# Optimization experiments

Measured on AMD Instinct MI355X. Metric: run time of the kernel, lower is better.

## Reference

```python
import jax, jax.numpy as jnp
import numpy as np

W_P, H_P = 2, 2  # patch rows, patch cols (size_of_patches[0])
HID, FC = 256, 1024

def _lstm_scan(x_seq, k, r, b):
    """Keras-style LSTM. x_seq: [T, N, Din] -> hidden states [T, N, H]."""
    N = x_seq.shape[1]
    H = r.shape[0]
    h0 = jnp.zeros((N, H), x_seq.dtype)
    c0 = jnp.zeros((N, H), x_seq.dtype)
    def step(carry, x):
        h, c = carry
        z = x @ k + h @ r + b  # [N, 4H], gate order i,f,g,o (keras)
        i, f, g, o = jnp.split(z, 4, axis=-1)
        c = jax.nn.sigmoid(f) * c + jax.nn.sigmoid(i) * jnp.tanh(g)
        h = jax.nn.sigmoid(o) * jnp.tanh(c)
        return (h, c), h
    _, hs = jax.lax.scan(step, (h0, c0), x_seq)
    return hs

def _bidir(x, k_f, r_f, b_f, k_b, r_b, b_b):
    # x: [T, N, D] -> [T, N, 2H]
    hf = _lstm_scan(x, k_f, r_f, b_f)
    hb = _lstm_scan(x[::-1], k_b, r_b, b_b)[::-1]
    return jnp.concatenate([hf, hb], axis=-1)

def reference(x, k_ud, r_ud, b_ud, k_du, r_du, b_du,
              k_lr, r_lr, b_lr, k_rl, r_rl, b_rl, Wd, bd):
    B, Hi, Wi, C = x.shape
    I, J = Hi // W_P, Wi // H_P
    # extract non-overlapping patches -> [B, I, J, w_p*h_p*C]
    p = x.reshape(B, I, W_P, J, H_P, C).transpose(0, 1, 3, 2, 4, 5)
    p = p.reshape(B, I, J, W_P * H_P * C)
    # vertical bidirectional sweep: sequence over rows i, batched over (B, J)
    v = p.transpose(1, 0, 2, 3).reshape(I, B * J, -1)          # [I, B*J, D]
    v = _bidir(v, k_ud, r_ud, b_ud, k_du, r_du, b_du)          # [I, B*J, 2H]
    v = v.reshape(I, B, J, -1).transpose(1, 0, 2, 3)           # [B, I, J, 2H]
    # horizontal bidirectional sweep: sequence over cols j, batched over (B, I)
    h = v.transpose(2, 0, 1, 3).reshape(J, B * I, -1)          # [J, B*I, 2H]
    h = _bidir(h, k_lr, r_lr, b_lr, k_rl, r_rl, b_rl)          # [J, B*I, 2H]
    h = h.reshape(J, B, I, -1).transpose(1, 2, 0, 3)           # [B, I, J, 2H]
    return jax.nn.relu(h @ Wd + bd)                            # [B, I, J, FC]

def setup_inputs() -> dict:
    key = jax.random.key(0)
    ks = jax.random.split(key, 16)
    D = W_P * H_P * 3
    def n(k, shape):
        return jax.random.normal(k, shape, dtype=jnp.float32) * 0.05
    inp = {"x": jax.random.normal(ks[0], (64, 64, 64, 3), dtype=jnp.float32)}
    for idx, (name, din) in enumerate([("ud", D), ("du", D), ("lr", 2 * HID), ("rl", 2 * HID)]):
        inp[f"k_{name}"] = n(ks[1 + 3 * idx], (din, 4 * HID))
        inp[f"r_{name}"] = n(ks[2 + 3 * idx], (HID, 4 * HID))
        inp[f"b_{name}"] = jnp.zeros((4 * HID,), jnp.float32)
    inp["Wd"] = n(ks[13], (2 * HID, FC))
    inp["bd"] = jnp.zeros((FC,), jnp.float32)
    return inp
```

## Files before the change

### kernel.cpp

```cpp
#include <hip/hip_runtime.h>
#include <math.h>
#include <stddef.h>
#include <stdint.h>


namespace {

typedef __bf16 bf16x8 __attribute__((ext_vector_type(8)));
typedef float f32x4 __attribute__((ext_vector_type(4)));
typedef __attribute__((address_space(1))) unsigned int as1_uint;
typedef __attribute__((address_space(3))) unsigned int as3_uint;

__device__ __forceinline__ float bf2f(ushort u) {
  return __builtin_bit_cast(float, (unsigned int)u << 16);
}
__device__ __forceinline__ ushort f2bf(float f) {
  unsigned int u = __builtin_bit_cast(unsigned int, f);
  u += 0x7fffu + ((u >> 16) & 1u);
  return (ushort)(u >> 16);
}
__device__ __forceinline__ unsigned int packbf(float a, float b) {
  return (unsigned int)f2bf(a) | ((unsigned int)f2bf(b) << 16);
}
__device__ __forceinline__ float sigm(float x) {
  return __fdividef(1.f, 1.f + __expf(-x));
}
__device__ __forceinline__ float tanh_(float x) {
  return 2.f * sigm(2.f * x) - 1.f;
}
__device__ __forceinline__ f32x4 mfma16(bf16x8 a, bf16x8 b, f32x4 c) {
  return __builtin_amdgcn_mfma_f32_16x16x32_bf16(a, b, c, 0, 0, 0);
}
__device__ __forceinline__ void load_lds16(const void* g, void* l) {
  __builtin_amdgcn_global_load_lds((const as1_uint*)g, (as3_uint*)l, 16, 0, 0);
}


__global__ __launch_bounds__(256) void transpose_all(
    const float* __restrict__ s0, const float* __restrict__ s1,
    const float* __restrict__ s2, ushort* __restrict__ d0,
    ushort* __restrict__ d1, ushort* __restrict__ d2) {
  const int which = blockIdx.y;
  const float* in = (which == 0) ? s0 : (which == 1) ? s1 : s2;
  ushort* out = (which == 0) ? d0 : (which == 1) ? d1 : d2;
  const int idx = blockIdx.x * 256 + threadIdx.x;
  const int n = idx >> 9, k = idx & 511;
  out[idx] = f2bf(in[k * 1024 + n]);
}

__global__ __launch_bounds__(256) void rfrag_all(
    const float* __restrict__ r0, const float* __restrict__ r1,
    const float* __restrict__ r2, const float* __restrict__ r3,
    ushort* __restrict__ out) {
  const int which = blockIdx.y;
  const float* r = (which == 0) ? r0 : (which == 1) ? r1 : (which == 2) ? r2 : r3;
  ushort* o = out + (size_t)which * 262144;
  const int id = blockIdx.x * 256 + threadIdx.x;
  const int lane = id & 63, kc = (id >> 6) & 7, tile = id >> 9;
  const int kbase = (kc << 5) + ((lane >> 4) << 3);
  const int col = (tile << 4) + (lane & 15);
  ushort tmp[8];
#pragma unroll
  for (int j = 0; j < 8; ++j) tmp[j] = f2bf(r[(size_t)(kbase + j) * 1024 + col]);
  *(uint4*)&o[(size_t)id << 3] = *(const uint4*)tmp;
}

__global__ __launch_bounds__(256) void kfragv_kernel(
    const float* __restrict__ k0, const float* __restrict__ b0,
    const float* __restrict__ k1, const float* __restrict__ b1,
    ushort* __restrict__ out) {
  const int dir = blockIdx.y;
  const int idx = blockIdx.x * 256 + threadIdx.x;
  const int lane = idx & 63;
  const int kbase = (lane >> 4) << 3;
  const int col = ((idx >> 6) << 4) + (lane & 15);
  const float* kw = dir ? k1 : k0;
  const float* bw = dir ? b1 : b0;
  ushort tmp[8];
#pragma unroll
  for (int j = 0; j < 8; ++j) {
    const int kidx = kbase + j;
    const float v = (kidx < 12) ? kw[kidx * 1024 + col]
                  : (kidx == 12) ? bw[col] : 0.f;
    tmp[j] = f2bf(v);
  }
  *(uint4*)&out[((size_t)dir * 4096 + idx) << 3] = *(const uint4*)tmp;
}

__global__ __launch_bounds__(512) void lstm_sweepV(
    const float* __restrict__ x, const ushort* __restrict__ kfragV,
    const uint4* __restrict__ rF, ushort* __restrict__ outbuf) {
  const int tid = threadIdx.x;
  const int lane = tid & 63, w = tid >> 6;
  const int l16 = lane & 15, kg = lane >> 4;
  const int rb = blockIdx.x, dir = (int)blockIdx.y;
  const int rowbase = rb << 4;
  const int bb = rb >> 1;
  const int jbase = (rb & 1) << 4;

  __shared__ ushort hbuf[2][4096];
  __shared__ uint4 kfr[4096];
  __shared__ ushort pb[2][512];

  const uint4* rFd = rF + (size_t)dir * 32768;

  for (int e = tid; e < 640; e += 512) {
    const int par = e / 320, rest = e - par * 320;
    const int row = rest / 20, c = 12 + rest % 20;
    pb[par][(row << 5) + c] = (c == 12) ? (ushort)0x3F80 : (ushort)0;
  }
  if (tid < 192) {
    const int row = tid / 12, d = tid - row * 12;
    const int pr = d / 6, rem = d - pr * 6, pc = rem / 3, c = rem - pc * 3;
    const int i0 = dir ? 31 : 0;
    const float v = x[((size_t)((bb * 64 + (i0 << 1) + pr) * 64) +
                       ((jbase + row) << 1) + pc) * 3 + c];
    pb[0][(row << 5) + d] = f2bf(v);
  }
#pragma unroll
  for (int i = 0; i < 8; ++i)
    load_lds16((const uint4*)kfragV + (size_t)dir * 4096 + tid + (i << 9),
               kfr + (tid - lane) + (i << 9));
  __syncthreads();

  float cst[2][4];
#pragma unroll
  for (int q = 0; q < 2; ++q)
#pragma unroll
    for (int r = 0; r < 4; ++r) cst[q][r] = 0.f;

  for (int t = 0; t < 32; ++t) {
    const int seq = dir ? (31 - t) : t;
    const ushort* hprev = hbuf[(t + 1) & 1];
    ushort* hnext = hbuf[t & 1];

    if (t) {
      const int seqP = dir ? (32 - t) : (t - 1);
      const int row = tid >> 5, c4o = tid & 31;
      const uint4 v = *(const uint4*)((const char*)hprev + row * 512 +
                                      ((c4o ^ (row & 7)) << 4));
      const int n = rowbase + row, b = n >> 5, sp = n & 31;
      *(uint4*)&outbuf[(((size_t)(b * 32 + seqP) * 32 + sp) << 9) +
                       (dir << 8) + (c4o << 3)] = v;
    }

    float pv = 0.f;
    if (t < 31 && tid < 192) {
      const int row = tid / 12, d = tid - row * 12;
      const int pr = d / 6, rem = d - pr * 6, pc = rem / 3, c = rem - pc * 3;
      const int iN = dir ? (30 - t) : (t + 1);
      pv = x[((size_t)((bb * 64 + (iN << 1) + pr) * 64) +
              ((jbase + row) << 1) + pc) * 3 + c];
    }

    const bf16x8 pf = __builtin_bit_cast(
        bf16x8, *(const uint4*)&pb[t & 1][(l16 << 5) + (kg << 3)]);
    f32x4 acc[2][4];
#pragma unroll
    for (int q = 0; q < 2; ++q) {
#pragma unroll
      for (int g = 0; g < 4; ++g) {
        const int tile = (g << 4) + (w << 1) + q;
        const bf16x8 kb = __builtin_bit_cast(bf16x8, kfr[(tile << 6) + lane]);
        acc[q][g] = mfma16(pf, kb, (f32x4){0.f, 0.f, 0.f, 0.f});
      }
    }

    if (t) {
#pragma unroll
      for (int q = 0; q < 2; ++q) {
        uint4 bfr[2][4];
#pragma unroll
        for (int g = 0; g < 4; ++g)
          bfr[0][g] = rFd[(size_t)(((g << 4) + (w << 1) + q) << 3) * 64 + lane];
#pragma unroll
        for (int kc = 0; kc < 8; ++kc) {
          const int cur = kc & 1;
          if (kc < 7) {
#pragma unroll
            for (int g = 0; g < 4; ++g)
              bfr[cur ^ 1][g] =
                  rFd[((size_t)(((g << 4) + (w << 1) + q) << 3) + kc + 1) * 64 +
                      lane];
          }
          const int c4 = (kc << 2) + kg;
          const uint4 a = *(const uint4*)((const char*)hprev + l16 * 512 +
                                          ((c4 ^ (l16 & 7)) << 4));
          const bf16x8 ab = __builtin_bit_cast(bf16x8, a);
#pragma unroll
          for (int g = 0; g < 4; ++g)
            acc[q][g] =
                mfma16(ab, __builtin_bit_cast(bf16x8, bfr[cur][g]), acc[q][g]);
        }
      }
    }

    if (t < 31 && tid < 192) {
      const int row = tid / 12, d = tid - row * 12;
      pb[(t + 1) & 1][(row << 5) + d] = f2bf(pv);
    }

#pragma unroll
    for (int q = 0; q < 2; ++q) {
      const int col = (w << 5) + (q << 4) + l16;
#pragma unroll
      for (int r = 0; r < 4; ++r) {
        const float zi = acc[q][0][r];
        const float zf = acc[q][1][r];
        const float zg = acc[q][2][r];
        const float zo = acc[q][3][r];
        const float cn = sigm(zf) * cst[q][r] + sigm(zi) * tanh_(zg);
        cst[q][r] = cn;
        const float hv = sigm(zo) * tanh_(cn);
        const int row = (kg << 2) + r;
        *(ushort*)((char*)hnext + row * 512 +
                   (((col >> 3) ^ (row & 7)) << 4) + ((col & 7) << 1)) =
            f2bf(hv);
      }
    }
    __syncthreads();
  }

  {
    const int seqP = dir ? 0 : 31;
    const ushort* hl = hbuf[1];
    const int row = tid >> 5, c4o = tid & 31;
    const uint4 v = *(const uint4*)((const char*)hl + row * 512 +
                                    ((c4o ^ (row & 7)) << 4));
    const int n = rowbase + row, b = n >> 5, sp = n & 31;
    *(uint4*)&outbuf[(((size_t)(b * 32 + seqP) * 32 + sp) << 9) + (dir << 8) +
                     (c4o << 3)] = v;
  }
}

__global__ __launch_bounds__(512) void lstm_sweep7(
    const uint4* __restrict__ Zf, const uint4* __restrict__ rF,
    ushort* __restrict__ outbuf, int vert) {
  const int tid = threadIdx.x;
  const int lane = tid & 63, w = tid >> 6;
  const int l16 = lane & 15, kg = lane >> 4;
  const int rb = blockIdx.x, dir = (int)blockIdx.y;
  const int rowbase = rb << 4;

  __shared__ ushort hbuf[2][4096];

  const uint4* rFd = rF + (size_t)dir * 32768;
  const uint4* zb = Zf + ((size_t)dir * 128 + rb) * 65536;

  float cst[2][4];
#pragma unroll
  for (int q = 0; q < 2; ++q)
#pragma unroll
    for (int r = 0; r < 4; ++r) cst[q][r] = 0.f;

  uint4 zA[2], zB[2];
  {
    const int seq0 = dir ? 31 : 0;
    zA[0] = zb[(size_t)(seq0 << 2) * 512 + tid];
    zA[1] = zb[(size_t)((seq0 << 2) + 1) * 512 + tid];
  }

  for (int t = 0; t < 32; ++t) {
    const ushort* hprev = hbuf[(t + 1) & 1];
    ushort* hnext = hbuf[t & 1];

    if (t) {
      const int seqP = dir ? (32 - t) : (t - 1);
      const int row = tid >> 5, c4 = tid & 31;
      const uint4 v = *(const uint4*)((const char*)hprev + row * 512 +
                                      ((c4 ^ (row & 7)) << 4));
      const int n = rowbase + row, b = n >> 5, sp = n & 31;
      const int X = vert ? seqP : sp, Y = vert ? sp : seqP;
      *(uint4*)&outbuf[(((size_t)(b * 32 + X) * 32 + Y) << 9) + (dir << 8) +
                       (c4 << 3)] = v;
    }

#pragma unroll
    for (int q = 0; q < 2; ++q) {
      uint4(&zc)[2] = (q == 0) ? zA : zB;
      uint4(&zn)[2] = (q == 0) ? zB : zA;

      f32x4 acc[4];
#pragma unroll
      for (int g = 0; g < 4; ++g) {
        const unsigned int u0 = (g == 0) ? zc[0].x : (g == 1) ? zc[0].y
                                : (g == 2) ? zc[0].z : zc[0].w;
        const unsigned int u1 = (g == 0) ? zc[1].x : (g == 1) ? zc[1].y
                                : (g == 2) ? zc[1].z : zc[1].w;
        acc[g][0] = bf2f((ushort)(u0 & 0xffffu));
        acc[g][1] = bf2f((ushort)(u0 >> 16));
        acc[g][2] = bf2f((ushort)(u1 & 0xffffu));
        acc[g][3] = bf2f((ushort)(u1 >> 16));
      }

      if (t) {
        uint4 bfr[2][4];
#pragma unroll
        for (int g = 0; g < 4; ++g)
          bfr[0][g] = rFd[(size_t)(((g << 4) + (w << 1) + q) << 3) * 64 + lane];
#pragma unroll
        for (int kc = 0; kc < 8; ++kc) {
          const int cur = kc & 1;
          if (kc < 7) {
#pragma unroll
            for (int g = 0; g < 4; ++g)
              bfr[cur ^ 1][g] =
                  rFd[((size_t)(((g << 4) + (w << 1) + q) << 3) + kc + 1) * 64 +
                      lane];
          }
          const int c4 = (kc << 2) + kg;
          const uint4 a = *(const uint4*)((const char*)hprev + l16 * 512 +
                                          ((c4 ^ (l16 & 7)) << 4));
          const bf16x8 ab = __builtin_bit_cast(bf16x8, a);
#pragma unroll
          for (int g = 0; g < 4; ++g)
            acc[g] = mfma16(ab, __builtin_bit_cast(bf16x8, bfr[cur][g]), acc[g]);
        }
      }

      if (t < 31 || q == 0) {
        const int tn = q ? (t + 1) : t;
        const int qn = q ^ 1;
        const int seqn = dir ? (31 - tn) : tn;
        zn[0] = zb[(size_t)(((seqn << 1) + qn) << 1) * 512 + tid];
        zn[1] = zb[(size_t)((((seqn << 1) + qn) << 1) + 1) * 512 + tid];
      }

      const int col = (w << 5) + (q << 4) + l16;
#pragma unroll
      for (int r = 0; r < 4; ++r) {
        const float zi = acc[0][r];
        const float zf = acc[1][r];
        const float zg = acc[2][r];
        const float zo = acc[3][r];
        const float cn = sigm(zf) * cst[q][r] + sigm(zi) * tanh_(zg);
        cst[q][r] = cn;
        const float hv = sigm(zo) * tanh_(cn);
        const int row = (kg << 2) + r;
        *(ushort*)((char*)hnext + row * 512 +
                   (((col >> 3) ^ (row & 7)) << 4) + ((col & 7) << 1)) =
            f2bf(hv);
      }
    }
    __syncthreads();
  }

  {
    const int seqP = dir ? 0 : 31;
    const ushort* hl = hbuf[1];
    const int row = tid >> 5, c4 = tid & 31;
    const uint4 v = *(const uint4*)((const char*)hl + row * 512 +
                                    ((c4 ^ (row & 7)) << 4));
    const int n = rowbase + row, b = n >> 5, sp = n & 31;
    const int X = vert ? seqP : sp, Y = vert ? sp : seqP;
    *(uint4*)&outbuf[(((size_t)(b * 32 + X) * 32 + Y) << 9) + (dir << 8) +
                     (c4 << 3)] = v;
  }
}

__global__ __launch_bounds__(512) void gemm_bt_dual(
    const ushort* __restrict__ A, const ushort* __restrict__ BT0,
    const ushort* __restrict__ BT1, const float* __restrict__ bias0,
    const float* __restrict__ bias1, uint4* __restrict__ Zf) {
  const int tid = threadIdx.x;
  const int lane = tid & 63, wid = tid >> 6;
  const int l16 = lane & 15, kg = lane >> 4;
  const int wr = wid >> 1, wc = wid & 1;
  const int bid = blockIdx.x;
  const int xcd = bid & 7, lid = bid >> 3;
  const int m0 = ((xcd << 6) + (lid >> 4)) << 7;
  const int nb = lid & 15;
  const int dirq = nb >> 3;
  const int hc0 = (nb & 7) << 5;
  const ushort* BT = dirq ? BT1 : BT0;
  const float* bias = dirq ? bias1 : bias0;
  uint4* Cz = Zf + (size_t)dirq * 8388608;

  union SM {
    struct { uint4 A[128][8]; uint4 B[128][8]; } k;
    ushort eh[128][136];
  };
  __shared__ SM sm;

  f32x4 acc[2][4];
#pragma unroll
  for (int mt = 0; mt < 2; ++mt)
#pragma unroll
    for (int nt = 0; nt < 4; ++nt) acc[mt][nt] = (f32x4){0.f, 0.f, 0.f, 0.f};

  for (int k0 = 0; k0 < 512; k0 += 64) {
#pragma unroll
    for (int c = 0; c < 2; ++c) {
      const int cid = (wid << 7) + (c << 6) + lane;
      const int row = cid >> 3, ch = cid & 7;
      const int sch = ch ^ (row & 7);
      const int brow = ((row >> 5) << 8) + hc0 + (row & 31);
      load_lds16(A + (size_t)(m0 + row) * 512 + k0 + (sch << 3),
                 (uint4*)sm.k.A + (cid - lane));
      load_lds16(BT + (size_t)brow * 512 + k0 + (sch << 3),
                 (uint4*)sm.k.B + (cid - lane));
    }
    __syncthreads();
#pragma unroll
    for (int kk = 0; kk < 2; ++kk) {
      const int q = (kk << 2) + kg;
      bf16x8 a[2], b[4];
#pragma unroll
      for (int mt = 0; mt < 2; ++mt) {
        const int rr = (wr << 5) + (mt << 4) + l16;
        a[mt] = __builtin_bit_cast(bf16x8, sm.k.A[rr][q ^ (rr & 7)]);
      }
#pragma unroll
      for (int nt = 0; nt < 4; ++nt) {
        const int rr = (wc << 6) + (nt << 4) + l16;
        b[nt] = __builtin_bit_cast(bf16x8, sm.k.B[rr][q ^ (rr & 7)]);
      }
#pragma unroll
      for (int mt = 0; mt < 2; ++mt)
#pragma unroll
        for (int nt = 0; nt < 4; ++nt)
          acc[mt][nt] = mfma16(a[mt], b[nt], acc[mt][nt]);
    }
    __syncthreads();
  }

  float bn[4];
#pragma unroll
  for (int nt = 0; nt < 4; ++nt) {
    const int lcol = (wc << 6) + (nt << 4) + l16;
    bn[nt] = bias[((lcol >> 5) << 8) + hc0 + (lcol & 31)];
  }

#pragma unroll
  for (int mt = 0; mt < 2; ++mt) {
#pragma unroll
    for (int nt = 0; nt < 4; ++nt) {
      const int col = (wc << 6) + (nt << 4) + l16;
#pragma unroll
      for (int r = 0; r < 4; ++r) {
        const int rowl = (wr << 5) + (mt << 4) + (kg << 2) + r;
        sm.eh[rowl][col] = f2bf(acc[mt][nt][r] + bn[nt]);
      }
    }
  }
  __syncthreads();

#pragma unroll
  for (int h = 0; h < 2; ++h) {
    const int n_a = ((m0 >> 6) + h) << 1;
    const int rbz = n_a >> 4;
    const int n2l = (n_a & 15) >> 1;
    const int kgz = n2l >> 1, pz = n2l & 1;
#pragma unroll
    for (int it = 0; it < 2; ++it) {
      const int e = tid + (it << 9);
      const int seq = e >> 5, hl = e & 31;
      const int qv = hl >> 4, l16v = hl & 15;
      const int wz = (hc0 + hl) >> 5;
      const int tidz = (wz << 6) + (kgz << 4) + l16v;
      uint4 o;
      o.x = (unsigned int)sm.eh[(h << 6) + seq][hl] |
            ((unsigned int)sm.eh[(h << 6) + 32 + seq][hl] << 16);
      o.y = (unsigned int)sm.eh[(h << 6) + seq][32 + hl] |
            ((unsigned int)sm.eh[(h << 6) + 32 + seq][32 + hl] << 16);
      o.z = (unsigned int)sm.eh[(h << 6) + seq][64 + hl] |
            ((unsigned int)sm.eh[(h << 6) + 32 + seq][64 + hl] << 16);
      o.w = (unsigned int)sm.eh[(h << 6) + seq][96 + hl] |
            ((unsigned int)sm.eh[(h << 6) + 32 + seq][96 + hl] << 16);
      Cz[(size_t)rbz * 65536 + (size_t)((((seq << 1) + qv) << 1) + pz) * 512 +
         tidz] = o;
    }
  }
}

__global__ __launch_bounds__(512) void gemm_dense(
    const ushort* __restrict__ A, const ushort* __restrict__ BT,
    const float* __restrict__ bias, float* __restrict__ out) {
  const int tid = threadIdx.x;
  const int lane = tid & 63, wid = tid >> 6;
  const int l16 = lane & 15, kg = lane >> 4;
  const int wr = wid >> 1, wc = wid & 1;
  const int bid = blockIdx.x;
  const int xcd = bid & 7, lid = bid >> 3;
  const int m0 = ((xcd << 6) + (lid >> 3)) << 7;
  const int n0 = (lid & 7) << 7;

  union SM {
    struct { uint4 A[128][8]; uint4 B[128][8]; } k;
    float ef[64][132];
  };
  __shared__ SM sm;

  f32x4 acc[2][4];
#pragma unroll
  for (int mt = 0; mt < 2; ++mt)
#pragma unroll
    for (int nt = 0; nt < 4; ++nt) acc[mt][nt] = (f32x4){0.f, 0.f, 0.f, 0.f};

  for (int k0 = 0; k0 < 512; k0 += 64) {
#pragma unroll
    for (int c = 0; c < 2; ++c) {
      const int cid = (wid << 7) + (c << 6) + lane;
      const int row = cid >> 3, ch = cid & 7;
      const int sch = ch ^ (row & 7);
      load_lds16(A + (size_t)(m0 + row) * 512 + k0 + (sch << 3),
                 (uint4*)sm.k.A + (cid - lane));
      load_lds16(BT + (size_t)(n0 + row) * 512 + k0 + (sch << 3),
                 (uint4*)sm.k.B + (cid - lane));
    }
    __syncthreads();
#pragma unroll
    for (int kk = 0; kk < 2; ++kk) {
      const int q = (kk << 2) + kg;
      bf16x8 a[2], b[4];
#pragma unroll
      for (int mt = 0; mt < 2; ++mt) {
        const int rr = (wr << 5) + (mt << 4) + l16;
        a[mt] = __builtin_bit_cast(bf16x8, sm.k.A[rr][q ^ (rr & 7)]);
      }
#pragma unroll
      for (int nt = 0; nt < 4; ++nt) {
        const int rr = (wc << 6) + (nt << 4) + l16;
        b[nt] = __builtin_bit_cast(bf16x8, sm.k.B[rr][q ^ (rr & 7)]);
      }
#pragma unroll
      for (int mt = 0; mt < 2; ++mt)
#pragma unroll
        for (int nt = 0; nt < 4; ++nt)
          acc[mt][nt] = mfma16(a[mt], b[nt], acc[mt][nt]);
    }
    __syncthreads();
  }

  float bn[4];
#pragma unroll
  for (int nt = 0; nt < 4; ++nt)
    bn[nt] = bias[n0 + (wc << 6) + (nt << 4) + l16];

#pragma unroll
  for (int h = 0; h < 2; ++h) {
    __syncthreads();
    if ((wr >> 1) == h) {
#pragma unroll
      for (int mt = 0; mt < 2; ++mt) {
#pragma unroll
        for (int nt = 0; nt < 4; ++nt) {
          const int col = (wc << 6) + (nt << 4) + l16;
#pragma unroll
          for (int r = 0; r < 4; ++r) {
            const int rowl = ((wr & 1) << 5) + (mt << 4) + (kg << 2) + r;
            sm.ef[rowl][col] = fmaxf(acc[mt][nt][r] + bn[nt], 0.f);
          }
        }
      }
    }
    __syncthreads();
#pragma unroll
    for (int it = 0; it < 4; ++it) {
      const int c = tid + (it << 9);
      const int row = c >> 5, co = (c & 31) << 2;
      const f32x4 v = *(const f32x4*)&sm.ef[row][co];
      __builtin_nontemporal_store(
          v, (f32x4*)(out + (size_t)(m0 + (h << 6) + row) * 1024 + n0 + co));
    }
  }
}

}

extern "C" void kernel_launch(void* const* d_in, const int* in_sizes, int n_in,
                              void* d_out, int out_size, void* d_ws, size_t ws_size,
                              hipStream_t stream) {
  (void)in_sizes; (void)n_in; (void)out_size; (void)ws_size;
  const float* x    = (const float*)d_in[0];
  const float* k_ud = (const float*)d_in[1];
  const float* r_ud = (const float*)d_in[2];
  const float* b_ud = (const float*)d_in[3];
  const float* k_du = (const float*)d_in[4];
  const float* r_du = (const float*)d_in[5];
  const float* b_du = (const float*)d_in[6];
  const float* k_lr = (const float*)d_in[7];
  const float* r_lr = (const float*)d_in[8];
  const float* b_lr = (const float*)d_in[9];
  const float* k_rl = (const float*)d_in[10];
  const float* r_rl = (const float*)d_in[11];
  const float* b_rl = (const float*)d_in[12];
  const float* Wd   = (const float*)d_in[13];
  const float* bd   = (const float*)d_in[14];

  ushort* W     = (ushort*)d_ws;
  ushort* Z     = W;
  ushort* vbuf  = Z + 134217728;
  ushort* rF    = vbuf + 33554432;
  ushort* kTh   = rF + 1048576;
  ushort* WdT   = kTh + 1048576;
  ushort* kfragV = WdT + 524288;
  uint4* Zf = (uint4*)Z;

  rfrag_all<<<dim3(128, 4), 256, 0, stream>>>(r_ud, r_du, r_lr, r_rl, rF);
  transpose_all<<<dim3(2048, 3), 256, 0, stream>>>(k_lr, k_rl, Wd, kTh,
                                                   kTh + 524288, WdT);
  kfragv_kernel<<<dim3(16, 2), 256, 0, stream>>>(k_ud, b_ud, k_du, b_du,
                                                 kfragV);

  lstm_sweepV<<<dim3(128, 2), 512, 0, stream>>>(x, kfragV, (const uint4*)rF,
                                                vbuf);

  gemm_bt_dual<<<8192, 512, 0, stream>>>(vbuf, kTh, kTh + 524288, b_lr, b_rl,
                                         Zf);

  lstm_sweep7<<<dim3(128, 2), 512, 0, stream>>>(
      Zf, (const uint4*)(rF + 524288), vbuf, 0);

  gemm_dense<<<4096, 512, 0, stream>>>(vbuf, WdT, bd, (float*)d_out);
}
```

Before: 716.4 us.

## Double-buffer GEMM K-tiles and keep one LSTM gate's recurrent weights in LDS

The two bf16 GEMM kernels (input projection and dense head) now use two LDS buffers per operand, loading the next 64-wide K tile while MFMAs run on the current one. This is meant to hide global-to-LDS load latency behind compute, at the cost of twice the LDS footprint. The horizontal LSTM sweep kernel preloads the input-gate slice of the recurrent weights (128 KB) into shared memory once, so each step reads only three gates' weights from global memory. That extra LDS limits occupancy to one block per CU. The double-buffered loop relies on the existing trailing barrier for correctness. Unused helpers and variables are also removed.

```diff
diff --git a/kernel.cpp b/kernel.cpp
--- a/kernel.cpp
+++ b/kernel.cpp
@@ -18,9 +18,6 @@
   unsigned int u = __builtin_bit_cast(unsigned int, f);
   u += 0x7fffu + ((u >> 16) & 1u);
   return (ushort)(u >> 16);
-}
-__device__ __forceinline__ unsigned int packbf(float a, float b) {
-  return (unsigned int)f2bf(a) | ((unsigned int)f2bf(b) << 16);
 }
 __device__ __forceinline__ float sigm(float x) {
   return __fdividef(1.f, 1.f + __expf(-x));
@@ -130,7 +127,6 @@
     for (int r = 0; r < 4; ++r) cst[q][r] = 0.f;
 
   for (int t = 0; t < 32; ++t) {
-    const int seq = dir ? (31 - t) : t;
     const ushort* hprev = hbuf[(t + 1) & 1];
     ushort* hnext = hbuf[t & 1];
 
@@ -243,9 +239,14 @@
   const int rowbase = rb << 4;
 
   __shared__ ushort hbuf[2][4096];
+  __shared__ uint4 rres[8192];
 
   const uint4* rFd = rF + (size_t)dir * 32768;
   const uint4* zb = Zf + ((size_t)dir * 128 + rb) * 65536;
+
+#pragma unroll
+  for (int i = 0; i < 16; ++i)
+    load_lds16(rFd + (i << 9) + tid, rres + (tid - lane) + (i << 9));
 
   float cst[2][4];
 #pragma unroll
@@ -294,17 +295,18 @@
       }
 
       if (t) {
-        uint4 bfr[2][4];
-#pragma unroll
-        for (int g = 0; g < 4; ++g)
-          bfr[0][g] = rFd[(size_t)(((g << 4) + (w << 1) + q) << 3) * 64 + lane];
+        uint4 bfr[2][3];
+#pragma unroll
+        for (int g = 1; g < 4; ++g)
+          bfr[0][g - 1] =
+              rFd[(size_t)(((g << 4) + (w << 1) + q) << 3) * 64 + lane];
 #pragma unroll
         for (int kc = 0; kc < 8; ++kc) {
           const int cur = kc & 1;
           if (kc < 7) {
 #pragma unroll
-            for (int g = 0; g < 4; ++g)
-              bfr[cur ^ 1][g] =
+            for (int g = 1; g < 4; ++g)
+              bfr[cur ^ 1][g - 1] =
                   rFd[((size_t)(((g << 4) + (w << 1) + q) << 3) + kc + 1) * 64 +
                       lane];
           }
@@ -312,9 +314,13 @@
           const uint4 a = *(const uint4*)((const char*)hprev + l16 * 512 +
                                           ((c4 ^ (l16 & 7)) << 4));
           const bf16x8 ab = __builtin_bit_cast(bf16x8, a);
-#pragma unroll
-          for (int g = 0; g < 4; ++g)
-            acc[g] = mfma16(ab, __builtin_bit_cast(bf16x8, bfr[cur][g]), acc[g]);
+          const bf16x8 b0 = __builtin_bit_cast(
+              bf16x8, rres[(size_t)(((((w << 1) + q) << 3) + kc) << 6) + lane]);
+          acc[0] = mfma16(ab, b0, acc[0]);
+#pragma unroll
+          for (int g = 1; g < 4; ++g)
+            acc[g] = mfma16(ab, __builtin_bit_cast(bf16x8, bfr[cur][g - 1]),
+                            acc[g]);
         }
       }
 
@@ -377,7 +383,7 @@
   uint4* Cz = Zf + (size_t)dirq * 8388608;
 
   union SM {
-    struct { uint4 A[128][8]; uint4 B[128][8]; } k;
+    struct { uint4 A[2][128][8]; uint4 B[2][128][8]; } k;
     ushort eh[128][136];
   };
   __shared__ SM sm;
@@ -388,7 +394,7 @@
 #pragma unroll
     for (int nt = 0; nt < 4; ++nt) acc[mt][nt] = (f32x4){0.f, 0.f, 0.f, 0.f};
 
-  for (int k0 = 0; k0 < 512; k0 += 64) {
+  auto STAGE = [&](int k0, int bi) {
 #pragma unroll
     for (int c = 0; c < 2; ++c) {
       const int cid = (wid << 7) + (c << 6) + lane;
@@ -396,11 +402,18 @@
       const int sch = ch ^ (row & 7);
       const int brow = ((row >> 5) << 8) + hc0 + (row & 31);
       load_lds16(A + (size_t)(m0 + row) * 512 + k0 + (sch << 3),
-                 (uint4*)sm.k.A + (cid - lane));
+                 (uint4*)sm.k.A[bi] + (cid - lane));
       load_lds16(BT + (size_t)brow * 512 + k0 + (sch << 3),
-                 (uint4*)sm.k.B + (cid - lane));
-    }
-    __syncthreads();
+                 (uint4*)sm.k.B[bi] + (cid - lane));
+    }
+  };
+
+  STAGE(0, 0);
+  __syncthreads();
+
+  for (int t = 0; t < 8; ++t) {
+    const int bi = t & 1;
+    if (t < 7) STAGE((t + 1) << 6, bi ^ 1);
 #pragma unroll
     for (int kk = 0; kk < 2; ++kk) {
       const int q = (kk << 2) + kg;
@@ -408,12 +421,12 @@
 #pragma unroll
       for (int mt = 0; mt < 2; ++mt) {
         const int rr = (wr << 5) + (mt << 4) + l16;
-        a[mt] = __builtin_bit_cast(bf16x8, sm.k.A[rr][q ^ (rr & 7)]);
+        a[mt] = __builtin_bit_cast(bf16x8, sm.k.A[bi][rr][q ^ (rr & 7)]);
       }
 #pragma unroll
       for (int nt = 0; nt < 4; ++nt) {
         const int rr = (wc << 6) + (nt << 4) + l16;
-        b[nt] = __builtin_bit_cast(bf16x8, sm.k.B[rr][q ^ (rr & 7)]);
+        b[nt] = __builtin_bit_cast(bf16x8, sm.k.B[bi][rr][q ^ (rr & 7)]);
       }
 #pragma unroll
       for (int mt = 0; mt < 2; ++mt)
@@ -486,7 +499,7 @@
   const int n0 = (lid & 7) << 7;
 
   union SM {
-    struct { uint4 A[128][8]; uint4 B[128][8]; } k;
+    struct { uint4 A[2][128][8]; uint4 B[2][128][8]; } k;
     float ef[64][132];
   };
   __shared__ SM sm;
@@ -497,18 +510,25 @@
 #pragma unroll
     for (int nt = 0; nt < 4; ++nt) acc[mt][nt] = (f32x4){0.f, 0.f, 0.f, 0.f};
 
-  for (int k0 = 0; k0 < 512; k0 += 64) {
+  auto STAGE = [&](int k0, int bi) {
 #pragma unroll
     for (int c = 0; c < 2; ++c) {
       const int cid = (wid << 7) + (c << 6) + lane;
       const int row = cid >> 3, ch = cid & 7;
       const int sch = ch ^ (row & 7);
       load_lds16(A + (size_t)(m0 + row) * 512 + k0 + (sch << 3),
-                 (uint4*)sm.k.A + (cid - lane));
+                 (uint4*)sm.k.A[bi] + (cid - lane));
       load_lds16(BT + (size_t)(n0 + row) * 512 + k0 + (sch << 3),
-                 (uint4*)sm.k.B + (cid - lane));
-    }
-    __syncthreads();
+                 (uint4*)sm.k.B[bi] + (cid - lane));
+    }
+  };
+
+  STAGE(0, 0);
+  __syncthreads();
+
+  for (int t = 0; t < 8; ++t) {
+    const int bi = t & 1;
+    if (t < 7) STAGE((t + 1) << 6, bi ^ 1);
 #pragma unroll
     for (int kk = 0; kk < 2; ++kk) {
       const int q = (kk << 2) + kg;
@@ -516,12 +536,12 @@
 #pragma unroll
       for (int mt = 0; mt < 2; ++mt) {
         const int rr = (wr << 5) + (mt << 4) + l16;
-        a[mt] = __builtin_bit_cast(bf16x8, sm.k.A[rr][q ^ (rr & 7)]);
+        a[mt] = __builtin_bit_cast(bf16x8, sm.k.A[bi][rr][q ^ (rr & 7)]);
       }
 #pragma unroll
       for (int nt = 0; nt < 4; ++nt) {
         const int rr = (wc << 6) + (nt << 4) + l16;
-        b[nt] = __builtin_bit_cast(bf16x8, sm.k.B[rr][q ^ (rr & 7)]);
+        b[nt] = __builtin_bit_cast(bf16x8, sm.k.B[bi][rr][q ^ (rr & 7)]);
       }
 #pragma unroll
       for (int mt = 0; mt < 2; ++mt)
```

New measurement: 694.0 us. 1.03x faster.
